# Kernel optimization log

Measured on AMD Instinct MI355X. Metric: run time of the kernel, lower is better.

The kernel has to match this reference:

```python
import jax, jax.numpy as jnp
import numpy as np

B, L, S, H, E = 4, 2048, 2048, 8, 64


def setup_inputs() -> dict:
    key = jax.random.key(0)
    kq, kk, kv, kt = jax.random.split(key, 4)
    queries = jax.random.normal(kq, (B, L, H, E), dtype=jnp.float32)
    keys = jax.random.normal(kk, (B, S, H, E), dtype=jnp.float32)
    values = jax.random.normal(kv, (B, S, H, E), dtype=jnp.float32)
    # de-stationarization log-scale factor, kept small so exp(tau) ~ O(1)
    tau = 0.1 * jax.random.normal(kt, (B, 1, 1, 1), dtype=jnp.float32)
    # causal mask: True above the diagonal (positions to be masked)
    attn_mask = jnp.triu(jnp.ones((L, S), dtype=bool), k=1)
    return {"queries": queries, "keys": keys, "values": values,
            "attn_mask": attn_mask, "tau": tau}


def reference(queries, keys, values, attn_mask, tau):
    # queries: [B,L,H,E], keys/values: [B,S,H,E], tau: [B,1,1,1], mask: [L,S]
    E_ = queries.shape[-1]
    scale = 1.0 / jnp.sqrt(jnp.asarray(E_, dtype=queries.dtype))
    # scores: [B,H,L,S], with tau-based de-stationarization rescale
    scores = jnp.einsum('blhe,bshe->bhls', queries, keys) * (scale * jnp.exp(tau))
    scores = jnp.where(attn_mask, -jnp.inf, scores)
    A = jax.nn.softmax(scores, axis=-1)  # dropout is identity at inference
    V = jnp.einsum('bhls,bshd->blhd', A, values)
    return V
```

## Files before the change

### kernel.cpp

```cpp
#include <hip/hip_runtime.h>
#include <hip/hip_bf16.h>
#include <math.h>

#define B_ 4
#define L_ 2048
#define H_ 8
#define E_ 64
#define HE 512

typedef short bf16x8 __attribute__((ext_vector_type(8)));
typedef float f32x4 __attribute__((ext_vector_type(4)));
typedef float f32x16 __attribute__((ext_vector_type(16)));
typedef unsigned short u16x4 __attribute__((ext_vector_type(4)));
typedef unsigned short u16x8 __attribute__((ext_vector_type(8)));

__device__ __forceinline__ unsigned short f2b(float f) {
  return __builtin_bit_cast(unsigned short, (__hip_bfloat16)f);
}
__device__ __forceinline__ unsigned cvtpk(float lo, float hi) {
  unsigned r;
  asm("v_cvt_pk_bf16_f32 %0, %1, %2" : "=v"(r) : "v"(lo), "v"(hi));
  return r;
}
__device__ __forceinline__ void pl32swap(unsigned &a, unsigned &b) {
  asm volatile("v_permlane32_swap_b32 %0, %1" : "+v"(a), "+v"(b));
}

__global__ __launch_bounds__(256, 2) void attn_fwd(
    const float* __restrict__ Q, const float* __restrict__ K,
    const float* __restrict__ V, const float* __restrict__ tau,
    float* __restrict__ O)
{
  const int f  = blockIdx.x + 16 * (blockIdx.y + 8 * blockIdx.z);
  const int u  = f >> 5, hb = f & 31;
  const int h  = hb & 7, b = hb >> 3;
  const int qt = (u < 8) ? u : 23 - u;

  const int tid  = threadIdx.x;
  const int wave = tid >> 6, lane = tid & 63;
  const int l31 = lane & 31, hi = lane >> 5;
  const int l7 = l31 & 7;

  __shared__ unsigned short ldsK[2][64 * 64];
  __shared__ unsigned short ldsV[2][64 * 64];

  const float qscale = 0.125f * expf(tau[b]) * 1.44269504088896f;
  const int q0w = qt * 128 + wave * 32;
  const int myq = q0w + l31;

  const float* Qb = Q + (((size_t)b * L_ + myq) * H_ + h) * E_;
  bf16x8 qf[4];
  #pragma unroll
  for (int ks = 0; ks < 4; ++ks) {
    f32x4 a = *(const f32x4*)(Qb + ks * 16 + hi * 8);
    f32x4 c = *(const f32x4*)(Qb + ks * 16 + hi * 8 + 4);
    #pragma unroll
    for (int j = 0; j < 4; ++j) {
      qf[ks][j]     = (short)f2b(a[j] * qscale);
      qf[ks][4 + j] = (short)f2b(c[j] * qscale);
    }
  }

  float m_run = -INFINITY, l_run = 0.0f;
  f32x16 oacc[2];
  #pragma unroll
  for (int nd = 0; nd < 2; ++nd)
    #pragma unroll
    for (int r = 0; r < 16; ++r) oacc[nd][r] = 0.0f;

  const int krow = tid >> 2, kcg = tid & 3;
  const int vkv = (tid & 15) * 4, vd = (tid >> 4) * 4;
  const float* Kp = K + ((size_t)b * L_ * H_ + h) * E_ + (size_t)krow * HE + kcg * 16;
  const float* Vp = V + ((size_t)b * L_ * H_ + h) * E_ + (size_t)vkv * HE + vd;
  const int kwo0 = krow * 64 + (((2 * kcg) ^ (krow & 7)) << 3);
  const int kwo1 = krow * 64 + (((2 * kcg + 1) ^ (krow & 7)) << 3);

  const int nt = 2 * qt + 2;
  const int tmaxw = 2 * qt + (wave >> 1);

  {
    f32x4 kq[4], vq[4];
    #pragma unroll
    for (int i = 0; i < 4; ++i) kq[i] = *(const f32x4*)(Kp + 4 * i);
    #pragma unroll
    for (int i = 0; i < 4; ++i) vq[i] = *(const f32x4*)(Vp + (size_t)i * HE);
    u16x8 w0, w1;
    #pragma unroll
    for (int j = 0; j < 4; ++j) {
      w0[j] = f2b(kq[0][j]); w0[4 + j] = f2b(kq[1][j]);
      w1[j] = f2b(kq[2][j]); w1[4 + j] = f2b(kq[3][j]);
    }
    *(u16x8*)(&ldsK[0][kwo0]) = w0;
    *(u16x8*)(&ldsK[0][kwo1]) = w1;
    #pragma unroll
    for (int jd = 0; jd < 4; ++jd) {
      const int row = vd + jd;
      u16x4 vw;
      #pragma unroll
      for (int i = 0; i < 4; ++i) vw[i] = f2b(vq[i][jd]);
      *(u16x4*)(&ldsV[0][row * 64 + (((vkv >> 3) ^ (row & 7)) << 3) + (vkv & 7)]) = vw;
    }
  }
  __syncthreads();
  int cur = 0;

  for (int t = 0; t < nt; ++t) {
    const bool havenext = (t + 1 < nt);
    f32x4 kq[4], vq[4];
    if (havenext) {
      const float* Kn = Kp + (size_t)(t + 1) * 64 * HE;
      const float* Vn = Vp + (size_t)(t + 1) * 64 * HE;
      #pragma unroll
      for (int i = 0; i < 4; ++i) kq[i] = *(const f32x4*)(Kn + 4 * i);
      #pragma unroll
      for (int i = 0; i < 4; ++i) vq[i] = *(const f32x4*)(Vn + (size_t)i * HE);
    }

    if (t <= tmaxw) {
      const unsigned short* Kl = ldsK[cur];
      const unsigned short* Vl = ldsV[cur];

      f32x16 sacc[2];
      #pragma unroll
      for (int mt = 0; mt < 2; ++mt)
        #pragma unroll
        for (int r = 0; r < 16; ++r) sacc[mt][r] = 0.0f;
      __builtin_amdgcn_s_setprio(1);
      #pragma unroll
      for (int ks = 0; ks < 4; ++ks) {
        #pragma unroll
        for (int mt = 0; mt < 2; ++mt) {
          bf16x8 kf = *(const bf16x8*)(Kl + (32 * mt + l31) * 64 +
                                       (((2 * ks + hi) ^ l7) << 3));
          sacc[mt] = __builtin_amdgcn_mfma_f32_32x32x16_bf16(kf, qf[ks], sacc[mt], 0, 0, 0);
        }
      }
      __builtin_amdgcn_s_setprio(0);

      if (t == tmaxw) {
        const int dq = myq - 64 * t;
        const int kvhi = 4 * hi;
        #pragma unroll
        for (int mt = 0; mt < 2; ++mt)
          #pragma unroll
          for (int r = 0; r < 16; ++r) {
            const int kvl = (r & 3) + 8 * (r >> 2) + 32 * mt;
            if (kvl + kvhi > dq) sacc[mt][r] = -3.0e38f;
          }
      }

      float p0 = sacc[0][0], p1 = sacc[0][1], p2 = sacc[0][2], p3 = sacc[0][3];
      #pragma unroll
      for (int mt = 0; mt < 2; ++mt)
        #pragma unroll
        for (int r = (mt == 0 ? 4 : 0); r < 16; r += 4) {
          p0 = fmaxf(p0, sacc[mt][r]);
          p1 = fmaxf(p1, sacc[mt][r + 1]);
          p2 = fmaxf(p2, sacc[mt][r + 2]);
          p3 = fmaxf(p3, sacc[mt][r + 3]);
        }
      float mx = fmaxf(fmaxf(p0, p1), fmaxf(p2, p3));
      mx = fmaxf(mx, __shfl_xor(mx, 32));

      if (!__all(mx - m_run <= 8.0f)) {
        const float mnew = fmaxf(m_run, mx);
        const float corr = exp2f(m_run - mnew);
        m_run = mnew;
        l_run *= corr;
        #pragma unroll
        for (int r = 0; r < 16; ++r) {
          const int qrow = (r & 3) + 8 * (r >> 2) + 4 * hi;
          const float cr = __shfl(corr, qrow);
          oacc[0][r] *= cr;
          oacc[1][r] *= cr;
        }
      }

      float s0 = 0.f, s1 = 0.f, s2 = 0.f, s3 = 0.f;
      #pragma unroll
      for (int mt = 0; mt < 2; ++mt)
        #pragma unroll
        for (int r = 0; r < 16; r += 4) {
          float e0 = exp2f(sacc[mt][r]     - m_run);
          float e1 = exp2f(sacc[mt][r + 1] - m_run);
          float e2 = exp2f(sacc[mt][r + 2] - m_run);
          float e3 = exp2f(sacc[mt][r + 3] - m_run);
          sacc[mt][r] = e0; sacc[mt][r + 1] = e1;
          sacc[mt][r + 2] = e2; sacc[mt][r + 3] = e3;
          s0 += e0; s1 += e1; s2 += e2; s3 += e3;
        }
      float rs = (s0 + s1) + (s2 + s3);
      rs += __shfl_xor(rs, 32);
      l_run += rs;

      unsigned pk0[8], pk1[8];
      #pragma unroll
      for (int i = 0; i < 8; ++i) pk0[i] = cvtpk(sacc[0][2 * i], sacc[0][2 * i + 1]);
      #pragma unroll
      for (int i = 0; i < 8; ++i) pk1[i] = cvtpk(sacc[1][2 * i], sacc[1][2 * i + 1]);
      bf16x8 pf[4];
      #pragma unroll
      for (int ks = 0; ks < 4; ++ks) {
        unsigned a  = (ks >> 1) ? pk1[4 * (ks & 1)]     : pk0[4 * (ks & 1)];
        unsigned y  = (ks >> 1) ? pk1[4 * (ks & 1) + 2] : pk0[4 * (ks & 1) + 2];
        unsigned a2 = (ks >> 1) ? pk1[4 * (ks & 1) + 1] : pk0[4 * (ks & 1) + 1];
        unsigned y2 = (ks >> 1) ? pk1[4 * (ks & 1) + 3] : pk0[4 * (ks & 1) + 3];
        pl32swap(a, y);
        pl32swap(a2, y2);
        union { unsigned w[4]; bf16x8 v; } pu;
        pu.w[0] = a; pu.w[1] = a2; pu.w[2] = y; pu.w[3] = y2;
        pf[ks] = pu.v;
      }

      __builtin_amdgcn_s_setprio(1);
      #pragma unroll
      for (int ks = 0; ks < 4; ++ks) {
        #pragma unroll
        for (int nd = 0; nd < 2; ++nd) {
          bf16x8 vf = *(const bf16x8*)(Vl + (32 * nd + l31) * 64 +
                                       (((2 * ks + hi) ^ l7) << 3));
          oacc[nd] = __builtin_amdgcn_mfma_f32_32x32x16_bf16(pf[ks], vf, oacc[nd], 0, 0, 0);
        }
      }
      __builtin_amdgcn_s_setprio(0);
    }

    if (havenext) {
      const int nb = cur ^ 1;
      u16x8 w0, w1;
      #pragma unroll
      for (int j = 0; j < 4; ++j) {
        w0[j] = f2b(kq[0][j]); w0[4 + j] = f2b(kq[1][j]);
        w1[j] = f2b(kq[2][j]); w1[4 + j] = f2b(kq[3][j]);
      }
      *(u16x8*)(&ldsK[nb][kwo0]) = w0;
      *(u16x8*)(&ldsK[nb][kwo1]) = w1;
      #pragma unroll
      for (int jd = 0; jd < 4; ++jd) {
        const int row = vd + jd;
        u16x4 vw;
        #pragma unroll
        for (int i = 0; i < 4; ++i) vw[i] = f2b(vq[i][jd]);
        *(u16x4*)(&ldsV[nb][row * 64 + (((vkv >> 3) ^ (row & 7)) << 3) + (vkv & 7)]) = vw;
      }
      __syncthreads();
      cur = nb;
    }
  }

  const float linv = 1.0f / l_run;
  float* Ob = O + (((size_t)b * L_ + q0w) * H_ + h) * E_;
  #pragma unroll
  for (int r = 0; r < 16; ++r) {
    const int qrow = (r & 3) + 8 * (r >> 2) + 4 * hi;
    const float inv = __shfl(linv, qrow);
    Ob[(size_t)qrow * HE + l31]      = oacc[0][r] * inv;
    Ob[(size_t)qrow * HE + 32 + l31] = oacc[1][r] * inv;
  }
}

extern "C" void kernel_launch(void* const* d_in, const int* in_sizes, int n_in,
                              void* d_out, int out_size, void* d_ws, size_t ws_size,
                              hipStream_t stream) {
  (void)in_sizes; (void)n_in; (void)out_size; (void)d_ws; (void)ws_size;
  const float* Q   = (const float*)d_in[0];
  const float* K   = (const float*)d_in[1];
  const float* V   = (const float*)d_in[2];
  const float* tau = (const float*)d_in[4];
  float* O = (float*)d_out;
  dim3 grid(L_ / 128, H_, B_), block(256);
  hipLaunchKernelGGL(attn_fwd, grid, block, 0, stream, Q, K, V, tau, O);
}
```

Measured before the change: 60.08 us.

## Balance causal attention work by splitting KV range and merging partials

Each block now handles two query tiles: query tile j over KV tiles 0..j, and query tile 15-j over the upper part of its KV range. This gives every block the same number of KV tiles, where before the busiest block set the critical path. The unnormalized partial outputs plus running max and sum are written to the output and a workspace. A second kernel merges them with log-sum-exp weights. In exchange it adds an extra launch and extra global traffic to write, reread and rewrite the full fp32 output, and it uses workspace memory.

```diff
diff --git a/kernel.cpp b/kernel.cpp
--- a/kernel.cpp
+++ b/kernel.cpp
@@ -29,12 +29,13 @@
 __global__ __launch_bounds__(256, 2) void attn_fwd(
     const float* __restrict__ Q, const float* __restrict__ K,
     const float* __restrict__ V, const float* __restrict__ tau,
-    float* __restrict__ O)
+    float* __restrict__ O, float* __restrict__ wsOB,
+    float* __restrict__ mA, float* __restrict__ lA,
+    float* __restrict__ mB, float* __restrict__ lB)
 {
   const int f  = blockIdx.x + 16 * (blockIdx.y + 8 * blockIdx.z);
-  const int u  = f >> 5, hb = f & 31;
+  const int j  = f >> 5, hb = f & 31;
   const int h  = hb & 7, b = hb >> 3;
-  const int qt = (u < 8) ? u : 23 - u;
 
   const int tid  = threadIdx.x;
   const int wave = tid >> 6, lane = tid & 63;
@@ -45,229 +46,247 @@
   __shared__ unsigned short ldsV[2][64 * 64];
 
   const float qscale = 0.125f * expf(tau[b]) * 1.44269504088896f;
-  const int q0w = qt * 128 + wave * 32;
-  const int myq = q0w + l31;
-
-  const float* Qb = Q + (((size_t)b * L_ + myq) * H_ + h) * E_;
-  bf16x8 qf[4];
-  #pragma unroll
-  for (int ks = 0; ks < 4; ++ks) {
-    f32x4 a = *(const f32x4*)(Qb + ks * 16 + hi * 8);
-    f32x4 c = *(const f32x4*)(Qb + ks * 16 + hi * 8 + 4);
-    #pragma unroll
-    for (int j = 0; j < 4; ++j) {
-      qf[ks][j]     = (short)f2b(a[j] * qscale);
-      qf[ks][4 + j] = (short)f2b(c[j] * qscale);
-    }
-  }
-
-  float m_run = -INFINITY, l_run = 0.0f;
-  f32x16 oacc[2];
-  #pragma unroll
-  for (int nd = 0; nd < 2; ++nd)
-    #pragma unroll
-    for (int r = 0; r < 16; ++r) oacc[nd][r] = 0.0f;
 
   const int krow = tid >> 2, kcg = tid & 3;
   const int vkv = (tid & 15) * 4, vd = (tid >> 4) * 4;
-  const float* Kp = K + ((size_t)b * L_ * H_ + h) * E_ + (size_t)krow * HE + kcg * 16;
-  const float* Vp = V + ((size_t)b * L_ * H_ + h) * E_ + (size_t)vkv * HE + vd;
-  const int kwo0 = krow * 64 + (((2 * kcg) ^ (krow & 7)) << 3);
+  const size_t bh = ((size_t)b * L_ * H_ + h) * E_;
+  const int kwo0 = krow * 64 + (((2 * kcg)     ^ (krow & 7)) << 3);
   const int kwo1 = krow * 64 + (((2 * kcg + 1) ^ (krow & 7)) << 3);
 
-  const int nt = 2 * qt + 2;
-  const int tmaxw = 2 * qt + (wave >> 1);
-
-  {
-    f32x4 kq[4], vq[4];
-    #pragma unroll
-    for (int i = 0; i < 4; ++i) kq[i] = *(const f32x4*)(Kp + 4 * i);
-    #pragma unroll
-    for (int i = 0; i < 4; ++i) vq[i] = *(const f32x4*)(Vp + (size_t)i * HE);
+  auto stage_write = [&](int nb, const f32x4 (&kq)[4], const f32x4 (&vq)[4]) {
     u16x8 w0, w1;
     #pragma unroll
-    for (int j = 0; j < 4; ++j) {
-      w0[j] = f2b(kq[0][j]); w0[4 + j] = f2b(kq[1][j]);
-      w1[j] = f2b(kq[2][j]); w1[4 + j] = f2b(kq[3][j]);
-    }
-    *(u16x8*)(&ldsK[0][kwo0]) = w0;
-    *(u16x8*)(&ldsK[0][kwo1]) = w1;
+    for (int jd = 0; jd < 4; ++jd) {
+      w0[jd] = f2b(kq[0][jd]); w0[4 + jd] = f2b(kq[1][jd]);
+      w1[jd] = f2b(kq[2][jd]); w1[4 + jd] = f2b(kq[3][jd]);
+    }
+    *(u16x8*)(&ldsK[nb][kwo0]) = w0;
+    *(u16x8*)(&ldsK[nb][kwo1]) = w1;
     #pragma unroll
     for (int jd = 0; jd < 4; ++jd) {
       const int row = vd + jd;
       u16x4 vw;
       #pragma unroll
       for (int i = 0; i < 4; ++i) vw[i] = f2b(vq[i][jd]);
-      *(u16x4*)(&ldsV[0][row * 64 + (((vkv >> 3) ^ (row & 7)) << 3) + (vkv & 7)]) = vw;
-    }
-  }
-  __syncthreads();
-  int cur = 0;
-
-  for (int t = 0; t < nt; ++t) {
-    const bool havenext = (t + 1 < nt);
-    f32x4 kq[4], vq[4];
-    if (havenext) {
-      const float* Kn = Kp + (size_t)(t + 1) * 64 * HE;
-      const float* Vn = Vp + (size_t)(t + 1) * 64 * HE;
-      #pragma unroll
-      for (int i = 0; i < 4; ++i) kq[i] = *(const f32x4*)(Kn + 4 * i);
-      #pragma unroll
-      for (int i = 0; i < 4; ++i) vq[i] = *(const f32x4*)(Vn + (size_t)i * HE);
-    }
-
-    if (t <= tmaxw) {
-      const unsigned short* Kl = ldsK[cur];
-      const unsigned short* Vl = ldsV[cur];
-
-      f32x16 sacc[2];
-      #pragma unroll
-      for (int mt = 0; mt < 2; ++mt)
-        #pragma unroll
-        for (int r = 0; r < 16; ++r) sacc[mt][r] = 0.0f;
-      __builtin_amdgcn_s_setprio(1);
-      #pragma unroll
-      for (int ks = 0; ks < 4; ++ks) {
-        #pragma unroll
-        for (int mt = 0; mt < 2; ++mt) {
-          bf16x8 kf = *(const bf16x8*)(Kl + (32 * mt + l31) * 64 +
-                                       (((2 * ks + hi) ^ l7) << 3));
-          sacc[mt] = __builtin_amdgcn_mfma_f32_32x32x16_bf16(kf, qf[ks], sacc[mt], 0, 0, 0);
-        }
-      }
-      __builtin_amdgcn_s_setprio(0);
-
-      if (t == tmaxw) {
-        const int dq = myq - 64 * t;
-        const int kvhi = 4 * hi;
-        #pragma unroll
-        for (int mt = 0; mt < 2; ++mt)
-          #pragma unroll
-          for (int r = 0; r < 16; ++r) {
-            const int kvl = (r & 3) + 8 * (r >> 2) + 32 * mt;
-            if (kvl + kvhi > dq) sacc[mt][r] = -3.0e38f;
-          }
-      }
-
-      float p0 = sacc[0][0], p1 = sacc[0][1], p2 = sacc[0][2], p3 = sacc[0][3];
-      #pragma unroll
-      for (int mt = 0; mt < 2; ++mt)
-        #pragma unroll
-        for (int r = (mt == 0 ? 4 : 0); r < 16; r += 4) {
-          p0 = fmaxf(p0, sacc[mt][r]);
-          p1 = fmaxf(p1, sacc[mt][r + 1]);
-          p2 = fmaxf(p2, sacc[mt][r + 2]);
-          p3 = fmaxf(p3, sacc[mt][r + 3]);
-        }
-      float mx = fmaxf(fmaxf(p0, p1), fmaxf(p2, p3));
-      mx = fmaxf(mx, __shfl_xor(mx, 32));
-
-      if (!__all(mx - m_run <= 8.0f)) {
-        const float mnew = fmaxf(m_run, mx);
-        const float corr = exp2f(m_run - mnew);
-        m_run = mnew;
-        l_run *= corr;
-        #pragma unroll
-        for (int r = 0; r < 16; ++r) {
-          const int qrow = (r & 3) + 8 * (r >> 2) + 4 * hi;
-          const float cr = __shfl(corr, qrow);
-          oacc[0][r] *= cr;
-          oacc[1][r] *= cr;
-        }
-      }
-
-      float s0 = 0.f, s1 = 0.f, s2 = 0.f, s3 = 0.f;
-      #pragma unroll
-      for (int mt = 0; mt < 2; ++mt)
-        #pragma unroll
-        for (int r = 0; r < 16; r += 4) {
-          float e0 = exp2f(sacc[mt][r]     - m_run);
-          float e1 = exp2f(sacc[mt][r + 1] - m_run);
-          float e2 = exp2f(sacc[mt][r + 2] - m_run);
-          float e3 = exp2f(sacc[mt][r + 3] - m_run);
-          sacc[mt][r] = e0; sacc[mt][r + 1] = e1;
-          sacc[mt][r + 2] = e2; sacc[mt][r + 3] = e3;
-          s0 += e0; s1 += e1; s2 += e2; s3 += e3;
-        }
-      float rs = (s0 + s1) + (s2 + s3);
-      rs += __shfl_xor(rs, 32);
-      l_run += rs;
-
-      unsigned pk0[8], pk1[8];
-      #pragma unroll
-      for (int i = 0; i < 8; ++i) pk0[i] = cvtpk(sacc[0][2 * i], sacc[0][2 * i + 1]);
-      #pragma unroll
-      for (int i = 0; i < 8; ++i) pk1[i] = cvtpk(sacc[1][2 * i], sacc[1][2 * i + 1]);
-      bf16x8 pf[4];
-      #pragma unroll
-      for (int ks = 0; ks < 4; ++ks) {
-        unsigned a  = (ks >> 1) ? pk1[4 * (ks & 1)]     : pk0[4 * (ks & 1)];
-        unsigned y  = (ks >> 1) ? pk1[4 * (ks & 1) + 2] : pk0[4 * (ks & 1) + 2];
-        unsigned a2 = (ks >> 1) ? pk1[4 * (ks & 1) + 1] : pk0[4 * (ks & 1) + 1];
-        unsigned y2 = (ks >> 1) ? pk1[4 * (ks & 1) + 3] : pk0[4 * (ks & 1) + 3];
-        pl32swap(a, y);
-        pl32swap(a2, y2);
-        union { unsigned w[4]; bf16x8 v; } pu;
-        pu.w[0] = a; pu.w[1] = a2; pu.w[2] = y; pu.w[3] = y2;
-        pf[ks] = pu.v;
-      }
-
-      __builtin_amdgcn_s_setprio(1);
-      #pragma unroll
-      for (int ks = 0; ks < 4; ++ks) {
-        #pragma unroll
-        for (int nd = 0; nd < 2; ++nd) {
-          bf16x8 vf = *(const bf16x8*)(Vl + (32 * nd + l31) * 64 +
-                                       (((2 * ks + hi) ^ l7) << 3));
-          oacc[nd] = __builtin_amdgcn_mfma_f32_32x32x16_bf16(pf[ks], vf, oacc[nd], 0, 0, 0);
-        }
-      }
-      __builtin_amdgcn_s_setprio(0);
-    }
-
-    if (havenext) {
-      const int nb = cur ^ 1;
-      u16x8 w0, w1;
-      #pragma unroll
-      for (int j = 0; j < 4; ++j) {
-        w0[j] = f2b(kq[0][j]); w0[4 + j] = f2b(kq[1][j]);
-        w1[j] = f2b(kq[2][j]); w1[4 + j] = f2b(kq[3][j]);
-      }
-      *(u16x8*)(&ldsK[nb][kwo0]) = w0;
-      *(u16x8*)(&ldsK[nb][kwo1]) = w1;
+      *(u16x4*)(&ldsV[nb][row * 64 + (((vkv >> 3) ^ (row & 7)) << 3) + (vkv & 7)]) = vw;
+    }
+  };
+  auto load_tile = [&](int t, f32x4 (&kq)[4], f32x4 (&vq)[4]) {
+    const float* Kn = K + bh + (size_t)(64 * t + krow) * HE + kcg * 16;
+    const float* Vn = V + bh + (size_t)(64 * t + vkv) * HE + vd;
+    #pragma unroll
+    for (int i = 0; i < 4; ++i) kq[i] = *(const f32x4*)(Kn + 4 * i);
+    #pragma unroll
+    for (int i = 0; i < 4; ++i) vq[i] = *(const f32x4*)(Vn + (size_t)i * HE);
+  };
+
+  auto run_phase = [&](int jj, int t0, int t1,
+                       float* Opart, float* mout, float* lout) {
+    const int q0w = jj * 128 + wave * 32;
+    const int myq = q0w + l31;
+    const int tmaxw = 2 * jj + (wave >> 1);
+
+    const float* Qb = Q + (((size_t)b * L_ + myq) * H_ + h) * E_;
+    bf16x8 qf[4];
+    #pragma unroll
+    for (int ks = 0; ks < 4; ++ks) {
+      f32x4 a = *(const f32x4*)(Qb + ks * 16 + hi * 8);
+      f32x4 c = *(const f32x4*)(Qb + ks * 16 + hi * 8 + 4);
       #pragma unroll
       for (int jd = 0; jd < 4; ++jd) {
-        const int row = vd + jd;
-        u16x4 vw;
-        #pragma unroll
-        for (int i = 0; i < 4; ++i) vw[i] = f2b(vq[i][jd]);
-        *(u16x4*)(&ldsV[nb][row * 64 + (((vkv >> 3) ^ (row & 7)) << 3) + (vkv & 7)]) = vw;
+        qf[ks][jd]     = (short)f2b(a[jd] * qscale);
+        qf[ks][4 + jd] = (short)f2b(c[jd] * qscale);
       }
-      __syncthreads();
-      cur = nb;
-    }
-  }
-
-  const float linv = 1.0f / l_run;
-  float* Ob = O + (((size_t)b * L_ + q0w) * H_ + h) * E_;
+    }
+
+    float m_run = -INFINITY, l_run = 0.0f;
+    f32x16 oacc[2];
+    #pragma unroll
+    for (int nd = 0; nd < 2; ++nd)
+      #pragma unroll
+      for (int r = 0; r < 16; ++r) oacc[nd][r] = 0.0f;
+
+    f32x4 kq[4], vq[4];
+    __syncthreads();
+    load_tile(t0, kq, vq);
+    stage_write(0, kq, vq);
+    __syncthreads();
+    int cur = 0;
+
+    for (int t = t0; t < t1; ++t) {
+      const bool havenext = (t + 1 < t1);
+      if (havenext) load_tile(t + 1, kq, vq);
+
+      if (t <= tmaxw) {
+        const unsigned short* Kl = ldsK[cur];
+        const unsigned short* Vl = ldsV[cur];
+
+        f32x16 sacc[2];
+        #pragma unroll
+        for (int mt = 0; mt < 2; ++mt)
+          #pragma unroll
+          for (int r = 0; r < 16; ++r) sacc[mt][r] = 0.0f;
+        __builtin_amdgcn_s_setprio(1);
+        #pragma unroll
+        for (int ks = 0; ks < 4; ++ks) {
+          #pragma unroll
+          for (int mt = 0; mt < 2; ++mt) {
+            bf16x8 kf = *(const bf16x8*)(Kl + (32 * mt + l31) * 64 +
+                                         (((2 * ks + hi) ^ l7) << 3));
+            sacc[mt] = __builtin_amdgcn_mfma_f32_32x32x16_bf16(kf, qf[ks], sacc[mt], 0, 0, 0);
+          }
+        }
+        __builtin_amdgcn_s_setprio(0);
+
+        if (t == tmaxw) {
+          const int dq = myq - 64 * t;
+          #pragma unroll
+          for (int mt = 0; mt < 2; ++mt)
+            #pragma unroll
+            for (int r = 0; r < 16; ++r) {
+              const int kvl = 32 * mt + (r & 3) + 8 * (r >> 2) + 4 * hi;
+              if (kvl > dq) sacc[mt][r] = -3.0e38f;
+            }
+        }
+
+        float p0 = sacc[0][0], p1 = sacc[0][1], p2 = sacc[0][2], p3 = sacc[0][3];
+        #pragma unroll
+        for (int mt = 0; mt < 2; ++mt)
+          #pragma unroll
+          for (int r = (mt == 0 ? 4 : 0); r < 16; r += 4) {
+            p0 = fmaxf(p0, sacc[mt][r]);
+            p1 = fmaxf(p1, sacc[mt][r + 1]);
+            p2 = fmaxf(p2, sacc[mt][r + 2]);
+            p3 = fmaxf(p3, sacc[mt][r + 3]);
+          }
+        float mx = fmaxf(fmaxf(p0, p1), fmaxf(p2, p3));
+        mx = fmaxf(mx, __shfl_xor(mx, 32));
+
+        if (!__all(mx - m_run <= 8.0f)) {
+          const float mnew = fmaxf(m_run, mx);
+          const float corr = exp2f(m_run - mnew);
+          m_run = mnew;
+          l_run *= corr;
+          #pragma unroll
+          for (int r = 0; r < 16; ++r) {
+            const int qrow = (r & 3) + 8 * (r >> 2) + 4 * hi;
+            const float cr = __shfl(corr, qrow);
+            oacc[0][r] *= cr;
+            oacc[1][r] *= cr;
+          }
+        }
+
+        float s0 = 0.f, s1 = 0.f, s2 = 0.f, s3 = 0.f;
+        #pragma unroll
+        for (int mt = 0; mt < 2; ++mt)
+          #pragma unroll
+          for (int r = 0; r < 16; r += 4) {
+            float e0 = exp2f(sacc[mt][r]     - m_run);
+            float e1 = exp2f(sacc[mt][r + 1] - m_run);
+            float e2 = exp2f(sacc[mt][r + 2] - m_run);
+            float e3 = exp2f(sacc[mt][r + 3] - m_run);
+            sacc[mt][r] = e0; sacc[mt][r + 1] = e1;
+            sacc[mt][r + 2] = e2; sacc[mt][r + 3] = e3;
+            s0 += e0; s1 += e1; s2 += e2; s3 += e3;
+          }
+        float rs = (s0 + s1) + (s2 + s3);
+        rs += __shfl_xor(rs, 32);
+        l_run += rs;
+
+        unsigned pk[2][8];
+        #pragma unroll
+        for (int mt = 0; mt < 2; ++mt)
+          #pragma unroll
+          for (int i = 0; i < 8; ++i)
+            pk[mt][i] = cvtpk(sacc[mt][2 * i], sacc[mt][2 * i + 1]);
+
+        __builtin_amdgcn_s_setprio(1);
+        #pragma unroll
+        for (int ks = 0; ks < 4; ++ks) {
+          const int c = ks & 1, mtx = ks >> 1;
+          unsigned a  = pk[mtx][4 * c];
+          unsigned y  = pk[mtx][4 * c + 2];
+          unsigned a2 = pk[mtx][4 * c + 1];
+          unsigned y2 = pk[mtx][4 * c + 3];
+          pl32swap(a, y);
+          pl32swap(a2, y2);
+          union { unsigned w[4]; bf16x8 v; } pu;
+          pu.w[0] = a; pu.w[1] = a2; pu.w[2] = y; pu.w[3] = y2;
+          #pragma unroll
+          for (int nd = 0; nd < 2; ++nd) {
+            bf16x8 vf = *(const bf16x8*)(Vl + (32 * nd + l31) * 64 +
+                                         (((2 * ks + hi) ^ l7) << 3));
+            oacc[nd] = __builtin_amdgcn_mfma_f32_32x32x16_bf16(pu.v, vf, oacc[nd], 0, 0, 0);
+          }
+        }
+        __builtin_amdgcn_s_setprio(0);
+      }
+
+      if (havenext) {
+        stage_write(cur ^ 1, kq, vq);
+        __syncthreads();
+        cur ^= 1;
+      }
+    }
+
+    float* Ob = Opart + (((size_t)b * L_ + q0w) * H_ + h) * E_;
+    #pragma unroll
+    for (int r = 0; r < 16; ++r) {
+      const int qrow = (r & 3) + 8 * (r >> 2) + 4 * hi;
+      Ob[(size_t)qrow * HE + l31]      = oacc[0][r];
+      Ob[(size_t)qrow * HE + 32 + l31] = oacc[1][r];
+    }
+    if (hi == 0) {
+      const int qh = (b * L_ + q0w + l31) * H_ + h;
+      mout[qh] = m_run;
+      lout[qh] = l_run;
+    }
+  };
+
+  run_phase(j, 0, j + 1, O, mA, lA);
+  run_phase(15 - j, 16 - j, 32 - 2 * j, wsOB, mB, lB);
+}
+
+__global__ __launch_bounds__(256) void attn_combine(
+    float* __restrict__ O, const float* __restrict__ wsOB,
+    const float* __restrict__ mA, const float* __restrict__ lA,
+    const float* __restrict__ mB, const float* __restrict__ lB)
+{
+  const int idx = blockIdx.x * 256 + threadIdx.x;
+  const int qh = idx >> 4;
+  const float ma = mA[qh], la = lA[qh];
+  const float mb = mB[qh], lb = lB[qh];
+  const float m = fmaxf(ma, mb);
+  const float wa = exp2f(ma - m), wb = exp2f(mb - m);
+  const float inv = 1.0f / (wa * la + wb * lb);
+  const f32x4 oa = ((const f32x4*)O)[idx];
+  const f32x4 ob = ((const f32x4*)wsOB)[idx];
+  f32x4 out;
   #pragma unroll
-  for (int r = 0; r < 16; ++r) {
-    const int qrow = (r & 3) + 8 * (r >> 2) + 4 * hi;
-    const float inv = __shfl(linv, qrow);
-    Ob[(size_t)qrow * HE + l31]      = oacc[0][r] * inv;
-    Ob[(size_t)qrow * HE + 32 + l31] = oacc[1][r] * inv;
-  }
+  for (int i = 0; i < 4; ++i) out[i] = (oa[i] * wa + ob[i] * wb) * inv;
+  ((f32x4*)O)[idx] = out;
 }
 
 extern "C" void kernel_launch(void* const* d_in, const int* in_sizes, int n_in,
                               void* d_out, int out_size, void* d_ws, size_t ws_size,
                               hipStream_t stream) {
-  (void)in_sizes; (void)n_in; (void)out_size; (void)d_ws; (void)ws_size;
+  (void)in_sizes; (void)n_in; (void)out_size; (void)ws_size;
   const float* Q   = (const float*)d_in[0];
   const float* K   = (const float*)d_in[1];
   const float* V   = (const float*)d_in[2];
   const float* tau = (const float*)d_in[4];
   float* O = (float*)d_out;
-  dim3 grid(L_ / 128, H_, B_), block(256);
-  hipLaunchKernelGGL(attn_fwd, grid, block, 0, stream, Q, K, V, tau, O);
-}
+
+  float* wsOB = (float*)d_ws;
+  float* mA = wsOB + (size_t)B_ * L_ * H_ * E_;
+  float* lA = mA + (size_t)B_ * L_ * H_;
+  float* mB = lA + (size_t)B_ * L_ * H_;
+  float* lB = mB + (size_t)B_ * L_ * H_;
+
+  dim3 grid(16, 8, 4), block(256);
+  hipLaunchKernelGGL(attn_fwd, grid, block, 0, stream,
+                     Q, K, V, tau, O, wsOB, mA, lA, mB, lB);
+  const int total4 = B_ * L_ * H_ * E_ / 4;
+  hipLaunchKernelGGL(attn_combine, dim3(total4 / 256), dim3(256), 0, stream,
+                     O, wsOB, mA, lA, mB, lB);
+}
```

New measurement: 59.56 us. Within noise of the previous version (-0.9%).
